# Kernel optimization log

Hardware: AMD Instinct MI355X
Metric: run time of the kernel (lower is better)

## Reference

```python
import jax, jax.numpy as jnp
import numpy as np

B, N, FE, CIN, COUT, H = 4, 256, 8, 16, 16, 64


def setup_inputs() -> dict:
    key = jax.random.key(0)
    k0, k1, k2, k3, k4 = jax.random.split(key, 5)
    node_attr = jax.random.normal(k0, (B, N, CIN), dtype=jnp.float32)
    edge_adj = jax.random.normal(k1, (B, N, N, FE), dtype=jnp.float32)
    # edge-network MLP: FE -> H (ReLU) -> CIN*COUT
    W1 = jax.random.normal(k2, (FE, H), dtype=jnp.float32) * (1.0 / np.sqrt(FE))
    b1 = jnp.zeros((H,), dtype=jnp.float32)
    W2 = jax.random.normal(k3, (H, CIN * COUT), dtype=jnp.float32) * (1.0 / np.sqrt(H))
    b2 = jnp.zeros((CIN * COUT,), dtype=jnp.float32)
    bound = 1.0 / np.sqrt(CIN)
    root = jax.random.uniform(k4, (CIN, COUT), dtype=jnp.float32, minval=-bound, maxval=bound)
    return {"node_attr": node_attr, "edge_adj": edge_adj, "W1": W1, "b1": b1,
            "W2": W2, "b2": b2, "root": root}


def reference(node_attr, edge_adj, W1, b1, W2, b2, root):
    b, n = edge_adj.shape[0], edge_adj.shape[1]
    cin, cout = root.shape
    fe = edge_adj.shape[-1]
    # net over all N^2 edge features -> per-edge [Cin, Cout] weight matrices
    e = edge_adj.reshape(b, n * n, fe)
    h = jax.nn.relu(e @ W1 + b1)                       # [B, N*N, H]
    w = (h @ W2 + b2).reshape(b, n, n, cin, cout)      # [B, i, j, Cin, Cout]
    # gather index = scatter index = (k mod N): edge (i,j) reads node j,
    # scatter-sums into node j  =>  out[j] = sum_i x[j] @ W[i, j]
    msg = jnp.einsum('bjc,bijcd->bijd', node_attr, w)  # [B, i, j, Cout]
    out = msg.sum(axis=1)                              # [B, N, Cout]
    out = out + node_attr @ root                       # root/self term
    return out
```

## Files before the change

kernel.cpp:

```cpp
#include <hip/hip_runtime.h>

#define B_    4
#define N_    256
#define FE_   8
#define CIN_  16
#define COUT_ 16
#define H_    64


__global__ __launch_bounds__(256) void nnconv_fused(
    const float* __restrict__ node_attr,
    const float* __restrict__ edge_adj,
    const float* __restrict__ W1,
    const float* __restrict__ b1,
    const float* __restrict__ W2,
    const float* __restrict__ b2,
    const float* __restrict__ root,
    float* __restrict__ out)
{
    const int Bid = blockIdx.x;
    const int p   = (Bid & 7) * 128 + (Bid >> 3);
    const int b   = p >> 8;
    const int j   = p & 255;
    const int t    = threadIdx.x;
    const int lane = t & 63;
    const int w    = t >> 6;

    __shared__ float e_s[N_][FE_];
    __shared__ float hpart[4][H_];
    __shared__ float Hsum[H_];
    __shared__ float contrib[CIN_][COUT_];

    {
        const float4* src = (const float4*)(edge_adj +
            (((size_t)b * N_ + t) * N_ + j) * FE_);
        float4 a0 = src[0];
        float4 a1 = src[1];
        float4* dst = (float4*)(&e_s[t][0]);
        dst[0] = a0;
        dst[1] = a1;
    }

    float w1r[FE_];
    #pragma unroll
    for (int f = 0; f < FE_; ++f) w1r[f] = W1[f * H_ + lane];
    const float b1r = b1[lane];

    __syncthreads();

    float accA = 0.f, accB = 0.f;
    const int i0 = w * 64;
    #pragma unroll 8
    for (int k = 0; k < 64; k += 2) {
        const float4* ev0 = (const float4*)(&e_s[i0 + k][0]);
        const float4* ev1 = (const float4*)(&e_s[i0 + k + 1][0]);
        const float4 ea = ev0[0], eb = ev0[1];
        const float4 fa = ev1[0], fb = ev1[1];
        float v0 = b1r, v1 = b1r;
        v0 = fmaf(ea.x, w1r[0], v0);  v1 = fmaf(fa.x, w1r[0], v1);
        v0 = fmaf(ea.y, w1r[1], v0);  v1 = fmaf(fa.y, w1r[1], v1);
        v0 = fmaf(ea.z, w1r[2], v0);  v1 = fmaf(fa.z, w1r[2], v1);
        v0 = fmaf(ea.w, w1r[3], v0);  v1 = fmaf(fa.w, w1r[3], v1);
        v0 = fmaf(eb.x, w1r[4], v0);  v1 = fmaf(fb.x, w1r[4], v1);
        v0 = fmaf(eb.y, w1r[5], v0);  v1 = fmaf(fb.y, w1r[5], v1);
        v0 = fmaf(eb.z, w1r[6], v0);  v1 = fmaf(fb.z, w1r[6], v1);
        v0 = fmaf(eb.w, w1r[7], v0);  v1 = fmaf(fb.w, w1r[7], v1);
        accA += fmaxf(v0, 0.f);
        accB += fmaxf(v1, 0.f);
    }
    hpart[w][lane] = accA + accB;
    __syncthreads();

    if (t < H_) {
        Hsum[t] = hpart[0][t] + hpart[1][t] + hpart[2][t] + hpart[3][t];
    }
    __syncthreads();

    float s0 = 0.f, s1 = 0.f, s2 = 0.f, s3 = 0.f;
    #pragma unroll
    for (int hq = 0; hq < 16; ++hq) {
        const float4 hv = *(const float4*)(&Hsum[hq * 4]);
        s0 = fmaf(hv.x, W2[(hq * 4 + 0) * 256 + t], s0);
        s1 = fmaf(hv.y, W2[(hq * 4 + 1) * 256 + t], s1);
        s2 = fmaf(hv.z, W2[(hq * 4 + 2) * 256 + t], s2);
        s3 = fmaf(hv.w, W2[(hq * 4 + 3) * 256 + t], s3);
    }
    const float ws = (float)N_ * b2[t] + ((s0 + s1) + (s2 + s3));

    const int c = t >> 4;
    const int d = t & 15;
    const float nodec = node_attr[((size_t)b * N_ + j) * CIN_ + c];
    contrib[c][d] = nodec * (ws + root[t]);
    __syncthreads();

    if (t < COUT_) {
        float o = 0.f;
        #pragma unroll
        for (int cc = 0; cc < CIN_; ++cc) o += contrib[cc][t];
        out[((size_t)b * N_ + j) * COUT_ + t] = o;
    }
}

extern "C" void kernel_launch(void* const* d_in, const int* in_sizes, int n_in,
                              void* d_out, int out_size, void* d_ws, size_t ws_size,
                              hipStream_t stream) {
    const float* node_attr = (const float*)d_in[0];
    const float* edge_adj  = (const float*)d_in[1];
    const float* W1        = (const float*)d_in[2];
    const float* b1        = (const float*)d_in[3];
    const float* W2        = (const float*)d_in[4];
    const float* b2        = (const float*)d_in[5];
    const float* root      = (const float*)d_in[6];
    float* out = (float*)d_out;

    nnconv_fused<<<dim3(B_ * N_), dim3(256), 0, stream>>>(
        node_attr, edge_adj, W1, b1, W2, b2, root, out);
}
```

Before: 79.38 us.

## Process four destination nodes per block for contiguous edge feature loads

Each block now handles four adjacent destination nodes with 1024 threads, so each source row of the edge tensor is read as a 128-byte contiguous span instead of a 32-byte fragment. The per-node hidden-sum, W2 projection and output reduction are replicated per group within the block. The goal is better global memory coalescing on the dominant edge_adj read. In exchange there are fewer, larger blocks, which may reduce latency hiding, and possible LDS bank conflicts on the wider rows.

Measured after the change: 79.13 us. Within noise of the previous version (-0.3%).

```diff
diff --git a/kernel.cpp b/kernel.cpp
--- a/kernel.cpp
+++ b/kernel.cpp
@@ -6,9 +6,10 @@
 #define CIN_  16
 #define COUT_ 16
 #define H_    64
+#define JG_   4
 
 
-__global__ __launch_bounds__(256) void nnconv_fused(
+__global__ __launch_bounds__(1024) void nnconv_fused4(
     const float* __restrict__ node_attr,
     const float* __restrict__ edge_adj,
     const float* __restrict__ W1,
@@ -18,27 +19,28 @@
     const float* __restrict__ root,
     float* __restrict__ out)
 {
-    const int Bid = blockIdx.x;
-    const int p   = (Bid & 7) * 128 + (Bid >> 3);
-    const int b   = p >> 8;
-    const int j   = p & 255;
+    const int blk = blockIdx.x;
+    const int b   = blk >> 6;
+    const int j0  = (blk & 63) << 2;
     const int t    = threadIdx.x;
     const int lane = t & 63;
     const int w    = t >> 6;
 
-    __shared__ float e_s[N_][FE_];
-    __shared__ float hpart[4][H_];
-    __shared__ float Hsum[H_];
-    __shared__ float contrib[CIN_][COUT_];
+    __shared__ float e_s[N_][JG_ * FE_];
+    __shared__ float hpart[JG_][4][H_];
+    __shared__ float Hsum[JG_][H_];
+    __shared__ float contrib[JG_][CIN_][COUT_];
 
     {
-        const float4* src = (const float4*)(edge_adj +
-            (((size_t)b * N_ + t) * N_ + j) * FE_);
-        float4 a0 = src[0];
-        float4 a1 = src[1];
-        float4* dst = (float4*)(&e_s[t][0]);
-        dst[0] = a0;
-        dst[1] = a1;
+        const float4* eg = (const float4*)edge_adj;
+        float4* es4 = (float4*)(&e_s[0][0]);
+        const int q0 = t;
+        const int q1 = t + 1024;
+        const size_t base = (size_t)b * (N_ * 512) + j0 * 2;
+        float4 v0 = eg[base + (size_t)(q0 >> 3) * 512 + (q0 & 7)];
+        float4 v1 = eg[base + (size_t)(q1 >> 3) * 512 + (q1 & 7)];
+        es4[q0] = v0;
+        es4[q1] = v1;
     }
 
     float w1r[FE_];
@@ -48,12 +50,13 @@
 
     __syncthreads();
 
+    const int g  = w & 3;
+    const int i0 = (w >> 2) << 6;
     float accA = 0.f, accB = 0.f;
-    const int i0 = w * 64;
     #pragma unroll 8
     for (int k = 0; k < 64; k += 2) {
-        const float4* ev0 = (const float4*)(&e_s[i0 + k][0]);
-        const float4* ev1 = (const float4*)(&e_s[i0 + k + 1][0]);
+        const float4* ev0 = (const float4*)(&e_s[i0 + k][g * FE_]);
+        const float4* ev1 = (const float4*)(&e_s[i0 + k + 1][g * FE_]);
         const float4 ea = ev0[0], eb = ev0[1];
         const float4 fa = ev1[0], fb = ev1[1];
         float v0 = b1r, v1 = b1r;
@@ -68,36 +71,41 @@
         accA += fmaxf(v0, 0.f);
         accB += fmaxf(v1, 0.f);
     }
-    hpart[w][lane] = accA + accB;
+    hpart[g][w >> 2][lane] = accA + accB;
     __syncthreads();
 
-    if (t < H_) {
-        Hsum[t] = hpart[0][t] + hpart[1][t] + hpart[2][t] + hpart[3][t];
+    if (t < JG_ * H_) {
+        const int gg = t >> 6, hh = t & 63;
+        Hsum[gg][hh] = hpart[gg][0][hh] + hpart[gg][1][hh]
+                     + hpart[gg][2][hh] + hpart[gg][3][hh];
     }
     __syncthreads();
 
+    const int g2 = t >> 8;
+    const int td = t & 255;
     float s0 = 0.f, s1 = 0.f, s2 = 0.f, s3 = 0.f;
     #pragma unroll
     for (int hq = 0; hq < 16; ++hq) {
-        const float4 hv = *(const float4*)(&Hsum[hq * 4]);
-        s0 = fmaf(hv.x, W2[(hq * 4 + 0) * 256 + t], s0);
-        s1 = fmaf(hv.y, W2[(hq * 4 + 1) * 256 + t], s1);
-        s2 = fmaf(hv.z, W2[(hq * 4 + 2) * 256 + t], s2);
-        s3 = fmaf(hv.w, W2[(hq * 4 + 3) * 256 + t], s3);
+        const float4 hv = *(const float4*)(&Hsum[g2][hq * 4]);
+        s0 = fmaf(hv.x, W2[(hq * 4 + 0) * 256 + td], s0);
+        s1 = fmaf(hv.y, W2[(hq * 4 + 1) * 256 + td], s1);
+        s2 = fmaf(hv.z, W2[(hq * 4 + 2) * 256 + td], s2);
+        s3 = fmaf(hv.w, W2[(hq * 4 + 3) * 256 + td], s3);
     }
-    const float ws = (float)N_ * b2[t] + ((s0 + s1) + (s2 + s3));
+    const float ws = (float)N_ * b2[td] + ((s0 + s1) + (s2 + s3));
 
-    const int c = t >> 4;
-    const int d = t & 15;
-    const float nodec = node_attr[((size_t)b * N_ + j) * CIN_ + c];
-    contrib[c][d] = nodec * (ws + root[t]);
+    const int c = td >> 4;
+    const int d = td & 15;
+    const float nodec = node_attr[((size_t)b * N_ + (j0 + g2)) * CIN_ + c];
+    contrib[g2][c][d] = nodec * (ws + root[td]);
     __syncthreads();
 
-    if (t < COUT_) {
+    if (t < JG_ * COUT_) {
+        const int gg = t >> 4, dd = t & 15;
         float o = 0.f;
         #pragma unroll
-        for (int cc = 0; cc < CIN_; ++cc) o += contrib[cc][t];
-        out[((size_t)b * N_ + j) * COUT_ + t] = o;
+        for (int cc = 0; cc < CIN_; ++cc) o += contrib[gg][cc][dd];
+        out[((size_t)b * N_ + (j0 + gg)) * COUT_ + dd] = o;
     }
 }
 
@@ -113,6 +121,6 @@
     const float* root      = (const float*)d_in[6];
     float* out = (float*)d_out;
 
-    nnconv_fused<<<dim3(B_ * N_), dim3(256), 0, stream>>>(
+    nnconv_fused4<<<dim3(B_ * (N_ / JG_)), dim3(1024), 0, stream>>>(
         node_attr, edge_adj, W1, b1, W2, b2, root, out);
 }
```
